# Performance work log

Measured on AMD Instinct MI355X. Metric: run time of the kernel, lower is better.

Reference implementation:

```python
import jax, jax.numpy as jnp
import numpy as np

IN_DIM = 256
OUT_DIM = 64
N = 8192
ALPHA = 0.2  # LeakyReLU negative slope
NEG_BIG = -9e15


def setup_inputs() -> dict:
    key = jax.random.key(0)
    k_h, k_A, k_W, k_a = jax.random.split(key, 4)
    h = jax.random.normal(k_h, (N, IN_DIM), dtype=jnp.float32)
    A = jax.random.randint(k_A, (N, N), 0, 2, dtype=jnp.int32)
    # xavier_uniform with gain=1.414
    gain = 1.414
    lim_W = gain * np.sqrt(6.0 / (IN_DIM + OUT_DIM))
    W = jax.random.uniform(k_W, (IN_DIM, OUT_DIM), minval=-lim_W, maxval=lim_W, dtype=jnp.float32)
    lim_a = gain * np.sqrt(6.0 / (2 * OUT_DIM + 1))
    a = jax.random.uniform(k_a, (2 * OUT_DIM, 1), minval=-lim_a, maxval=lim_a, dtype=jnp.float32)
    return {"h": h, "A": A, "W": W, "a": a}


def reference(h, A, W, a):
    # Wh: [N, d]
    Wh = h @ W
    # e_ij = leakyrelu([Wh_i || Wh_j] . a) = leakyrelu(Wh_i.a1 + Wh_j.a2)
    # -> avoid the O(N^2 * 2d) concat; compute rank-1 decomposition directly.
    a1 = a[:OUT_DIM, 0]   # [d]
    a2 = a[OUT_DIM:, 0]   # [d]
    f1 = Wh @ a1          # [N] contribution of source node i
    f2 = Wh @ a2          # [N] contribution of target node j
    e = jax.nn.leaky_relu(f1[:, None] + f2[None, :], negative_slope=ALPHA)  # [N, N]
    e = jnp.where(A > 0, e, NEG_BIG)
    attention = jax.nn.softmax(e, axis=1)  # [N, N]
    # dropout=0.0 (eval mode): identity
    h_prime = attention @ Wh               # [N, d]
    return jax.nn.elu(h_prime)             # concat=True -> ELU
```

## Files before the change

### kernel.cpp

```cpp
#include <hip/hip_runtime.h>
#include <math.h>
#include <stdint.h>

#define NV 8192
#define KD 256
#define DD 64
#define ALPHA 0.2f
#define TI 64
#define SPLIT 16
#define BLK 256

typedef _Float16 half8 __attribute__((ext_vector_type(8)));
typedef float floatx4 __attribute__((ext_vector_type(4)));

#define OFF_WHT  0
#define OFF_F1   (DD * NV / 2)
#define OFF_F2   (OFF_F1 + NV)
#define OFF_PACC (OFF_F2 + NV)

__global__ __launch_bounds__(256) void gat_pre(
    const float* __restrict__ h, const float* __restrict__ W,
    const float* __restrict__ a, ushort* __restrict__ whT,
    float* __restrict__ f1, float* __restrict__ f2) {
  __shared__ float hrow[16][KD];
  __shared__ ushort tw[DD][20];
  const int tid = threadIdx.x;
  const int i0 = blockIdx.x * 16;
#pragma unroll
  for (int u = 0; u < 4; ++u) {
    const int idx = tid + u * 256;
    const int row = idx >> 6, col = (idx & 63) * 4;
    *(float4*)&hrow[row][col] = *(const float4*)&h[(long long)(i0 + row) * KD + col];
  }
  __syncthreads();
  const int d = tid & 63;
  const int rg = tid >> 6;
  float wh[4] = {0.f, 0.f, 0.f, 0.f};
#pragma unroll 4
  for (int c = 0; c < KD; ++c) {
    const float wc = W[c * DD + d];
#pragma unroll
    for (int r = 0; r < 4; ++r) wh[r] += hrow[rg * 4 + r][c] * wc;
  }
  const float a1 = a[d], a2 = a[DD + d];
#pragma unroll
  for (int r = 0; r < 4; ++r) {
    float p1 = wh[r] * a1, p2 = wh[r] * a2;
#pragma unroll
    for (int off = 32; off > 0; off >>= 1) {
      p1 += __shfl_down(p1, off);
      p2 += __shfl_down(p2, off);
    }
    if (d == 0) { f1[i0 + rg * 4 + r] = p1; f2[i0 + rg * 4 + r] = p2; }
    union { _Float16 hf; ushort u; } cv;
    cv.hf = (_Float16)wh[r];
    tw[d][rg * 4 + r] = cv.u;
  }
  __syncthreads();
  if (tid < 128) {
    const int dd = tid >> 1, hf = tid & 1;
    *(uint4*)&whT[(long long)dd * NV + i0 + hf * 8] = *(uint4*)&tw[dd][hf * 8];
  }
}

__global__ __launch_bounds__(BLK) __attribute__((amdgpu_waves_per_eu(4, 8)))
void gat_main(
    const int* __restrict__ A, const ushort* __restrict__ whT,
    const float* __restrict__ f1, const float* __restrict__ f2,
    float* __restrict__ pacc, float* __restrict__ pl, int S) {
  __shared__ float f2_lds[NV / SPLIT];
  __shared__ float redf[4];

  const int tid = threadIdx.x;
  const int wave = tid >> 6, lane = tid & 63;
  const int m_ = lane & 15, quad = lane >> 4;
  const int tile = blockIdx.x & 127;
  const int s = blockIdx.x >> 7;
  const int i0 = tile * TI;
  const int jrange = NV / S;
  const int j0 = s * jrange;

  float m = -1e30f;
#pragma unroll
  for (int q = 0; q < NV / BLK; ++q) m = fmaxf(m, f2[tid + q * BLK]);
#pragma unroll
  for (int off = 32; off > 0; off >>= 1) m = fmaxf(m, __shfl_down(m, off));
  if (lane == 0) redf[wave] = m;

  for (int u = tid * 4; u < jrange; u += BLK * 4)
    *(float4*)&f2_lds[u] = *(const float4*)&f2[j0 + u];
  __syncthreads();

  const float mm = fmaxf(fmaxf(redf[0], redf[1]), fmaxf(redf[2], redf[3]));
  const int row = i0 + wave * 16 + m_;
  const float f1r = f1[row];
  const float xm = f1r + mm;
  const float Mr = fmaxf(xm, ALPHA * xm);

  floatx4 acc[4], accl;
#pragma unroll
  for (int nt = 0; nt < 4; ++nt) acc[nt] = (floatx4){0.f, 0.f, 0.f, 0.f};
  accl = (floatx4){0.f, 0.f, 0.f, 0.f};
  const half8 ones = {(_Float16)1.f, (_Float16)1.f, (_Float16)1.f, (_Float16)1.f,
                      (_Float16)1.f, (_Float16)1.f, (_Float16)1.f, (_Float16)1.f};

  const int* Arow = A + (long long)row * NV + j0 + quad * 8;
  const ushort* Bb = whT + j0 + quad * 8;

  for (int kb = 0; kb < jrange; kb += 32) {
    const int4 a0 = *(const int4*)(Arow + kb);
    const int4 a1 = *(const int4*)(Arow + kb + 4);
    half8 b0 = *(const half8*)(Bb + (long long)(0 * 16 + m_) * NV + kb);
    half8 b1 = *(const half8*)(Bb + (long long)(1 * 16 + m_) * NV + kb);
    half8 b2 = *(const half8*)(Bb + (long long)(2 * 16 + m_) * NV + kb);
    half8 b3 = *(const half8*)(Bb + (long long)(3 * 16 + m_) * NV + kb);

    const int kk = kb + quad * 8;
    const float4 q0 = *(const float4*)&f2_lds[kk];
    const float4 q1 = *(const float4*)&f2_lds[kk + 4];

    union { _Float16 hf[8]; half8 v; } wf;
#define WELT(slot, aval, f2val)                                        \
    { float x = f1r + (f2val); x = fmaxf(x, ALPHA * x);                \
      float w = ((aval) > 0) ? __expf(x - Mr) : 0.f;                   \
      wf.hf[slot] = (_Float16)w; }
    WELT(0, a0.x, q0.x) WELT(1, a0.y, q0.y)
    WELT(2, a0.z, q0.z) WELT(3, a0.w, q0.w)
    WELT(4, a1.x, q1.x) WELT(5, a1.y, q1.y)
    WELT(6, a1.z, q1.z) WELT(7, a1.w, q1.w)
#undef WELT

    acc[0] = __builtin_amdgcn_mfma_f32_16x16x32_f16(wf.v, b0, acc[0], 0, 0, 0);
    acc[1] = __builtin_amdgcn_mfma_f32_16x16x32_f16(wf.v, b1, acc[1], 0, 0, 0);
    acc[2] = __builtin_amdgcn_mfma_f32_16x16x32_f16(wf.v, b2, acc[2], 0, 0, 0);
    acc[3] = __builtin_amdgcn_mfma_f32_16x16x32_f16(wf.v, b3, acc[3], 0, 0, 0);
    accl   = __builtin_amdgcn_mfma_f32_16x16x32_f16(wf.v, ones, accl, 0, 0, 0);
  }

  if (m_ == 0) {
#pragma unroll
    for (int reg = 0; reg < 4; ++reg)
      pl[(long long)s * NV + i0 + wave * 16 + quad * 4 + reg] = accl[reg];
  }

#pragma unroll
  for (int reg = 0; reg < 4; ++reg) {
    const int i = i0 + wave * 16 + quad * 4 + reg;
    const long long base = ((long long)s * NV + i) * DD + m_;
#pragma unroll
    for (int nt = 0; nt < 4; ++nt) pacc[base + 16 * nt] = acc[nt][reg];
  }
}

__global__ __launch_bounds__(256) void gat_fin(const float* __restrict__ pacc,
                                               const float* __restrict__ pl,
                                               float* __restrict__ out, int S) {
  const int idx = blockIdx.x * 256 + threadIdx.x;
  const int i = idx >> 6;
  float sum = 0.f, l = 0.f;
  for (int q = 0; q < S; ++q) sum += pacc[(long long)q * (NV * DD) + idx];
  for (int q = 0; q < S; ++q) l += pl[q * NV + i];
  const float v = sum / l;
  out[idx] = v > 0.f ? v : expm1f(v);
}

extern "C" void kernel_launch(void* const* d_in, const int* in_sizes, int n_in,
                              void* d_out, int out_size, void* d_ws, size_t ws_size,
                              hipStream_t stream) {
  const float* h = (const float*)d_in[0];
  const int* A = (const int*)d_in[1];
  const float* W = (const float*)d_in[2];
  const float* a = (const float*)d_in[3];
  float* out = (float*)d_out;
  float* ws = (float*)d_ws;

  ushort* whT = (ushort*)(ws + OFF_WHT);
  float* f1 = ws + OFF_F1;
  float* f2 = ws + OFF_F2;
  float* pacc = ws + OFF_PACC;

  const int S = SPLIT;
  float* pl = pacc + (size_t)S * NV * DD;

  gat_pre<<<NV / 16, 256, 0, stream>>>(h, W, a, whT, f1, f2);
  gat_main<<<(NV / TI) * S, BLK, 0, stream>>>(A, whT, f1, f2, pacc, pl, S);
  gat_fin<<<NV * DD / 256, 256, 0, stream>>>(pacc, pl, out, S);
}
```

Baseline: 450.3 us.

## Hoist row-max into separate kernel, unroll main loop 2x with nontemporal A loads

```diff
diff --git a/kernel.cpp b/kernel.cpp
--- a/kernel.cpp
+++ b/kernel.cpp
@@ -12,11 +12,13 @@
 
 typedef _Float16 half8 __attribute__((ext_vector_type(8)));
 typedef float floatx4 __attribute__((ext_vector_type(4)));
+typedef int intx4 __attribute__((ext_vector_type(4)));
 
 #define OFF_WHT  0
 #define OFF_F1   (DD * NV / 2)
 #define OFF_F2   (OFF_F1 + NV)
-#define OFF_PACC (OFF_F2 + NV)
+#define OFF_M    (OFF_F2 + NV)
+#define OFF_PACC (OFF_M + NV)
 
 __global__ __launch_bounds__(256) void gat_pre(
     const float* __restrict__ h, const float* __restrict__ W,
@@ -63,13 +65,31 @@
   }
 }
 
+__global__ __launch_bounds__(256) void gat_maxm(
+    const float* __restrict__ f1, const float* __restrict__ f2,
+    float* __restrict__ M) {
+  __shared__ float red[4];
+  const int tid = threadIdx.x;
+  float m = -1e30f;
+  for (int j = tid; j < NV; j += 256) m = fmaxf(m, f2[j]);
+#pragma unroll
+  for (int off = 32; off > 0; off >>= 1) m = fmaxf(m, __shfl_down(m, off));
+  if ((tid & 63) == 0) red[tid >> 6] = m;
+  __syncthreads();
+  const float mm = fmaxf(fmaxf(red[0], red[1]), fmaxf(red[2], red[3]));
+  for (int i = tid; i < NV; i += 256) {
+    const float x = f1[i] + mm;
+    M[i] = fmaxf(x, ALPHA * x);
+  }
+}
+
 __global__ __launch_bounds__(BLK) __attribute__((amdgpu_waves_per_eu(4, 8)))
 void gat_main(
     const int* __restrict__ A, const ushort* __restrict__ whT,
-    const float* __restrict__ f1, const float* __restrict__ f2,
-    float* __restrict__ pacc, float* __restrict__ pl, int S) {
+    const float* __restrict__ f1, const float* __restrict__ Mv,
+    const float* __restrict__ f2, float* __restrict__ pacc,
+    float* __restrict__ pl, int S) {
   __shared__ float f2_lds[NV / SPLIT];
-  __shared__ float redf[4];
 
   const int tid = threadIdx.x;
   const int wave = tid >> 6, lane = tid & 63;
@@ -80,22 +100,13 @@
   const int jrange = NV / S;
   const int j0 = s * jrange;
 
-  float m = -1e30f;
-#pragma unroll
-  for (int q = 0; q < NV / BLK; ++q) m = fmaxf(m, f2[tid + q * BLK]);
-#pragma unroll
-  for (int off = 32; off > 0; off >>= 1) m = fmaxf(m, __shfl_down(m, off));
-  if (lane == 0) redf[wave] = m;
-
   for (int u = tid * 4; u < jrange; u += BLK * 4)
     *(float4*)&f2_lds[u] = *(const float4*)&f2[j0 + u];
-  __syncthreads();
-
-  const float mm = fmaxf(fmaxf(redf[0], redf[1]), fmaxf(redf[2], redf[3]));
+
   const int row = i0 + wave * 16 + m_;
   const float f1r = f1[row];
-  const float xm = f1r + mm;
-  const float Mr = fmaxf(xm, ALPHA * xm);
+  const float Mr = Mv[row];
+  __syncthreads();
 
   floatx4 acc[4], accl;
 #pragma unroll
@@ -104,37 +115,50 @@
   const half8 ones = {(_Float16)1.f, (_Float16)1.f, (_Float16)1.f, (_Float16)1.f,
                       (_Float16)1.f, (_Float16)1.f, (_Float16)1.f, (_Float16)1.f};
 
-  const int* Arow = A + (long long)row * NV + j0 + quad * 8;
-  const ushort* Bb = whT + j0 + quad * 8;
-
-  for (int kb = 0; kb < jrange; kb += 32) {
-    const int4 a0 = *(const int4*)(Arow + kb);
-    const int4 a1 = *(const int4*)(Arow + kb + 4);
-    half8 b0 = *(const half8*)(Bb + (long long)(0 * 16 + m_) * NV + kb);
-    half8 b1 = *(const half8*)(Bb + (long long)(1 * 16 + m_) * NV + kb);
-    half8 b2 = *(const half8*)(Bb + (long long)(2 * 16 + m_) * NV + kb);
-    half8 b3 = *(const half8*)(Bb + (long long)(3 * 16 + m_) * NV + kb);
+  const intx4* Arow = (const intx4*)(A + (long long)row * NV + j0 + quad * 8);
+  const ushort* Bb = whT + (long long)m_ * NV + j0 + quad * 8;
+
+  for (int kb = 0; kb < jrange; kb += 64) {
+    const intx4 a0 = __builtin_nontemporal_load(Arow + (kb >> 2));
+    const intx4 a1 = __builtin_nontemporal_load(Arow + (kb >> 2) + 1);
+    const intx4 a2 = __builtin_nontemporal_load(Arow + ((kb + 32) >> 2));
+    const intx4 a3 = __builtin_nontemporal_load(Arow + ((kb + 32) >> 2) + 1);
+    half8 b0[4], b1[4];
+#pragma unroll
+    for (int nt = 0; nt < 4; ++nt) {
+      b0[nt] = *(const half8*)(Bb + (long long)(nt * 16) * NV + kb);
+      b1[nt] = *(const half8*)(Bb + (long long)(nt * 16) * NV + kb + 32);
+    }
 
     const int kk = kb + quad * 8;
     const float4 q0 = *(const float4*)&f2_lds[kk];
     const float4 q1 = *(const float4*)&f2_lds[kk + 4];
-
-    union { _Float16 hf[8]; half8 v; } wf;
-#define WELT(slot, aval, f2val)                                        \
+    const float4 q2 = *(const float4*)&f2_lds[kk + 32];
+    const float4 q3 = *(const float4*)&f2_lds[kk + 36];
+
+    union { _Float16 hf[8]; half8 v; } wfa, wfb;
+#define WELT(dst, slot, aval, f2val)                                   \
     { float x = f1r + (f2val); x = fmaxf(x, ALPHA * x);                \
       float w = ((aval) > 0) ? __expf(x - Mr) : 0.f;                   \
-      wf.hf[slot] = (_Float16)w; }
-    WELT(0, a0.x, q0.x) WELT(1, a0.y, q0.y)
-    WELT(2, a0.z, q0.z) WELT(3, a0.w, q0.w)
-    WELT(4, a1.x, q1.x) WELT(5, a1.y, q1.y)
-    WELT(6, a1.z, q1.z) WELT(7, a1.w, q1.w)
+      dst.hf[slot] = (_Float16)w; }
+    WELT(wfa, 0, a0.x, q0.x) WELT(wfa, 1, a0.y, q0.y)
+    WELT(wfa, 2, a0.z, q0.z) WELT(wfa, 3, a0.w, q0.w)
+    WELT(wfa, 4, a1.x, q1.x) WELT(wfa, 5, a1.y, q1.y)
+    WELT(wfa, 6, a1.z, q1.z) WELT(wfa, 7, a1.w, q1.w)
+    WELT(wfb, 0, a2.x, q2.x) WELT(wfb, 1, a2.y, q2.y)
+    WELT(wfb, 2, a2.z, q2.z) WELT(wfb, 3, a2.w, q2.w)
+    WELT(wfb, 4, a3.x, q3.x) WELT(wfb, 5, a3.y, q3.y)
+    WELT(wfb, 6, a3.z, q3.z) WELT(wfb, 7, a3.w, q3.w)
 #undef WELT
 
-    acc[0] = __builtin_amdgcn_mfma_f32_16x16x32_f16(wf.v, b0, acc[0], 0, 0, 0);
-    acc[1] = __builtin_amdgcn_mfma_f32_16x16x32_f16(wf.v, b1, acc[1], 0, 0, 0);
-    acc[2] = __builtin_amdgcn_mfma_f32_16x16x32_f16(wf.v, b2, acc[2], 0, 0, 0);
-    acc[3] = __builtin_amdgcn_mfma_f32_16x16x32_f16(wf.v, b3, acc[3], 0, 0, 0);
-    accl   = __builtin_amdgcn_mfma_f32_16x16x32_f16(wf.v, ones, accl, 0, 0, 0);
+#pragma unroll
+    for (int nt = 0; nt < 4; ++nt)
+      acc[nt] = __builtin_amdgcn_mfma_f32_16x16x32_f16(wfa.v, b0[nt], acc[nt], 0, 0, 0);
+    accl = __builtin_amdgcn_mfma_f32_16x16x32_f16(wfa.v, ones, accl, 0, 0, 0);
+#pragma unroll
+    for (int nt = 0; nt < 4; ++nt)
+      acc[nt] = __builtin_amdgcn_mfma_f32_16x16x32_f16(wfb.v, b1[nt], acc[nt], 0, 0, 0);
+    accl = __builtin_amdgcn_mfma_f32_16x16x32_f16(wfb.v, ones, accl, 0, 0, 0);
   }
 
   if (m_ == 0) {
@@ -177,12 +201,14 @@
   ushort* whT = (ushort*)(ws + OFF_WHT);
   float* f1 = ws + OFF_F1;
   float* f2 = ws + OFF_F2;
+  float* Mv = ws + OFF_M;
   float* pacc = ws + OFF_PACC;
 
   const int S = SPLIT;
   float* pl = pacc + (size_t)S * NV * DD;
 
   gat_pre<<<NV / 16, 256, 0, stream>>>(h, W, a, whT, f1, f2);
-  gat_main<<<(NV / TI) * S, BLK, 0, stream>>>(A, whT, f1, f2, pacc, pl, S);
+  gat_maxm<<<1, 256, 0, stream>>>(f1, f2, Mv);
+  gat_main<<<(NV / TI) * S, BLK, 0, stream>>>(A, whT, f1, Mv, f2, pacc, pl, S);
   gat_fin<<<NV * DD / 256, 256, 0, stream>>>(pacc, pl, out, S);
 }
```

Result: slower. 480.7 us (+6.7%).
